# Optimization experiments

Measured on AMD Instinct MI355X. Metric: run time of the kernel, lower is better.

Reference implementation:

```python
import jax, jax.numpy as jnp
import numpy as np

MIN_MAP = jnp.array([-3.602826, -3.602826, -3.602826], dtype=jnp.float32)

def _conv(x, w, stride, pad):
    return jax.lax.conv_general_dilated(x, w, (stride, stride), [(pad, pad), (pad, pad)],
                                        dimension_numbers=('NCHW', 'OIHW', 'NCHW'))

def _bn(x, g, b):
    # inference BatchNorm with running_mean=0, running_var=1 -> pure channel affine
    return x * g[None, :, None, None] + b[None, :, None, None]

def _maxpool2(x):
    return jax.lax.reduce_window(x, -jnp.inf, jax.lax.max, (1, 1, 2, 2), (1, 1, 2, 2), 'VALID')

def _rotations(angles):
    # angles: [N,3] (already multiplied by pi); matrix entries copied verbatim from the torch source
    c, s = jnp.cos(angles), jnp.sin(angles)
    z = jnp.zeros_like(c[:, 0]); o = jnp.ones_like(c[:, 0])
    Rx = jnp.stack([jnp.stack([o, z, z], -1),
                    jnp.stack([z, c[:, 0], s[:, 0]], -1),
                    jnp.stack([z, -s[:, 0], c[:, 0]], -1)], 1)
    Ry = jnp.stack([jnp.stack([c[:, 1], z, -s[:, 1]], -1),
                    jnp.stack([z, o, z], -1),
                    jnp.stack([s[:, 1], z, c[:, 1]], -1)], 1)
    Rz = jnp.stack([jnp.stack([c[:, 2], s[:, 2], z], -1),
                    jnp.stack([-s[:, 2], c[:, 2], z], -1),
                    jnp.stack([z, z, o], -1)], 1)
    return jnp.einsum('nij,njk,nkl->nil', Rx, Ry, Rz)  # [N,3,3]


def setup_inputs() -> dict:
    key = jax.random.key(0)
    ks = jax.random.split(key, 16)
    N, C, T, V, M = 32, 3, 224, 224, 2
    OC = 128
    def he(k, shape, fan_in):
        return jax.random.normal(k, shape, jnp.float32) * np.float32(np.sqrt(2.0 / fan_in))
    inp = {}
    inp['x'] = jax.random.normal(ks[0], (N, C, T, V, M), jnp.float32)
    inp['w1'] = he(ks[1], (OC, C, 5, 5), C * 25); inp['b1'] = jnp.zeros((OC,), jnp.float32)
    inp['g1'] = jnp.ones((OC,), jnp.float32); inp['be1'] = jnp.zeros((OC,), jnp.float32)
    inp['w2'] = he(ks[2], (OC, OC, 5, 5), OC * 25); inp['b2'] = jnp.zeros((OC,), jnp.float32)
    inp['g2'] = jnp.ones((OC,), jnp.float32); inp['be2'] = jnp.zeros((OC,), jnp.float32)
    feat = OC * (224 // 8) * (224 // 8)  # 100352
    inp['fw'] = jax.random.normal(ks[3], (6, feat), jnp.float32) * np.float32(np.sqrt(1.0 / feat))
    inp['fb'] = jnp.zeros((6,), jnp.float32)
    chans = [3, 64, 256, 512, 1024, 2048]  # surrogate ResNet-50-style /32 backbone
    for i in range(5):
        cin, cout = chans[i], chans[i + 1]
        inp['bw%d' % (i + 1)] = he(ks[4 + i], (cout, cin, 3, 3), cin * 9)
        inp['bg%d' % (i + 1)] = jnp.ones((cout,), jnp.float32)
        inp['bb%d' % (i + 1)] = jnp.zeros((cout,), jnp.float32)
    lin = 2048 * 7 * 7
    inp['lw'] = jax.random.normal(ks[10], (60, lin), jnp.float32) * np.float32(np.sqrt(1.0 / lin))
    inp['lb'] = jnp.zeros((60,), jnp.float32)
    return inp


def reference(x, w1, b1, g1, be1, w2, b2, g2, be2, fw, fb,
              bw1, bg1, bb1, bw2, bg2, bb2, bw3, bg3, bb3, bw4, bg4, bb4, bw5, bg5, bb5,
              lw, lb):
    N = x.shape[0]
    def person(xp):  # xp: [N,3,T,V]
        h = jax.nn.relu(_bn(_conv(xp, w1, 2, 2) + b1[None, :, None, None], g1, be1))
        h = jax.nn.relu(_bn(_conv(h, w2, 2, 2) + b2[None, :, None, None], g2, be2))
        h = _maxpool2(h)                       # [N,128,28,28]
        o = h.reshape(N, -1) @ fw.T + fb       # [N,6]
        # torch builds rotations from out[n,:3].item() -> constants w.r.t. autodiff
        R = _rotations(jax.lax.stop_gradient(o[:, :3]) * jnp.pi)
        xf = xp.reshape(N, 3, -1)
        rot = jnp.einsum('nij,njk->nik', R, xf)
        shift = jnp.einsum('nij,nj->ni', R, MIN_MAP[None, :] - o[:, 3:])
        bias = 255.0 * (shift - MIN_MAP[None, :]) / 8.812765
        z = (rot + bias[:, :, None]).reshape(xp.shape)
        for w, g, b in ((bw1, bg1, bb1), (bw2, bg2, bb2), (bw3, bg3, bb3),
                        (bw4, bg4, bb4), (bw5, bg5, bb5)):
            z = jax.nn.relu(_bn(_conv(z, w, 2, 1), g, b))
        return z  # [N,2048,7,7]
    out = jnp.maximum(person(x[..., 0]), person(x[..., 1]))
    return out.reshape(N, -1) @ lw.T + lb  # [N,60]
```

## Files before the change

### kernel.cpp

```cpp
#include <hip/hip_runtime.h>
#include <hip/hip_bf16.h>

typedef unsigned short u16;
typedef __attribute__((ext_vector_type(8))) short bf16x8;
typedef __attribute__((ext_vector_type(4))) float f32x4;
typedef __attribute__((ext_vector_type(8))) unsigned short u16x8;
typedef __attribute__((ext_vector_type(4))) unsigned short u16x4;

__device__ __forceinline__ u16 f2bf(float v) {
    __hip_bfloat16 b = __float2bfloat16(v);
    return *reinterpret_cast<u16*>(&b);
}
__device__ __forceinline__ float bf2f(u16 u) {
    __hip_bfloat16 b;
    *reinterpret_cast<u16*>(&b) = u;
    return __bfloat162float(b);
}

__device__ __forceinline__ void gl_lds16(const u16* g, u16* l) {
    __builtin_amdgcn_global_load_lds(
        (const __attribute__((address_space(1))) void*)g,
        (__attribute__((address_space(3))) void*)l, 16, 0, 0);
}

__global__ void repack_w32(const float* __restrict__ w, u16* __restrict__ wh,
                           int Cout, int Cin, int KK) {
    int i = blockIdx.x * blockDim.x + threadIdx.x;
    int tot = Cout * Cin * KK;
    if (i >= tot) return;
    int oc = i / (Cin * KK);
    int r = i - oc * (Cin * KK);
    int p = r / Cin, ic = r - p * Cin;
    wh[(size_t)oc * (Cin * KK) + (size_t)p * Cin + ic] =
        f2bf(w[((size_t)oc * Cin + ic) * KK + p]);
}
__global__ void repack_split2(const float* __restrict__ w, u16* __restrict__ Ap,
                              int Cout, int CinR, int CinP, int KK, int Ksteps) {
    int cols = Ksteps * 64;
    int idx = blockIdx.x * blockDim.x + threadIdx.x;
    int tot = Cout * cols;
    if (idx >= tot) return;
    int oc = idx / cols, c = idx - oc * cols;
    int t = c >> 6, r = c & 63, half = r >> 5, j = r & 31;
    int kk = t * 32 + j;
    int p = kk / CinP, ic = kk - p * CinP;
    float v = (p < KK && ic < CinR) ? w[((size_t)oc * CinR + ic) * KK + p] : 0.f;
    u16 h = f2bf(v);
    Ap[idx] = half ? f2bf(v - bf2f(h)) : h;
}
__global__ void repack_g4_2(const float* __restrict__ w, u16* __restrict__ Ap,
                            int Cout, int CinR, int KS, int Ksteps) {
    int cols = Ksteps * 64;
    int idx = blockIdx.x * blockDim.x + threadIdx.x;
    int tot = Cout * cols;
    if (idx >= tot) return;
    int oc = idx / cols, c = idx - oc * cols;
    int t = c >> 6, r = c & 63, half = r >> 5, j = r & 31;
    int pix = j >> 2, ch = j & 3;
    float v = (pix < KS && ch < CinR)
                  ? w[(((size_t)oc * CinR + ch) * KS + t) * KS + pix] : 0.f;
    u16 h = f2bf(v);
    Ap[idx] = half ? f2bf(v - bf2f(h)) : h;
}
__global__ void repack_g4(const float* __restrict__ w, u16* __restrict__ Ap,
                          int Cout, int CinR, int KS, int Kpp) {
    int idx = blockIdx.x * blockDim.x + threadIdx.x;
    int tot = Cout * Kpp;
    if (idx >= tot) return;
    int oc = idx / Kpp, kk = idx - oc * Kpp;
    int ky = kk >> 5, r = kk & 31;
    int pix = r >> 2, ch = r & 3;
    float v = (pix < KS && ch < CinR)
                  ? w[(((size_t)oc * CinR + ch) * KS + ky) * KS + pix] : 0.f;
    Ap[idx] = f2bf(v);
}

__global__ void extract_person4(const float* __restrict__ x, float* __restrict__ X,
                                u16* __restrict__ X4, int m, int total) {
    int idx = blockIdx.x * blockDim.x + threadIdx.x;
    if (idx >= total) return;
    int n = idx / 50176;
    int p = idx - n * 50176;
    int y = p / 224, xx = p - y * 224;
    u16 h[4];
    h[3] = 0;
#pragma unroll
    for (int c = 0; c < 3; ++c) {
        float v = x[(((size_t)(n * 3 + c)) * 50176 + p) * 2 + m];
        X[((size_t)(n * 3 + c)) * 50176 + p] = v;
        h[c] = f2bf(v);
    }
    size_t o = (((size_t)n * 228 + y + 2) * 232 + xx + 2) * 4;
    *reinterpret_cast<u16x4*>(&X4[o]) = *reinterpret_cast<u16x4*>(h);
}

__global__ void zero_u16(u16* __restrict__ b, size_t n8) {
    size_t i = (size_t)blockIdx.x * blockDim.x + threadIdx.x;
    if (i >= n8) return;
    u16x8 z = {0, 0, 0, 0, 0, 0, 0, 0};
    *reinterpret_cast<u16x8*>(&b[i * 8]) = z;
}
__global__ void zero_halo(u16* __restrict__ buf, int Nn, int Hp, int Wp, int C,
                          int P, int H, int W) {
    int idx = blockIdx.x * blockDim.x + threadIdx.x;
    int tot = Nn * Hp * Wp;
    if (idx >= tot) return;
    int x = idx % Wp, t = idx / Wp, y = t % Hp;
    if (y >= P && y < P + H && x >= P && x < P + W) return;
    u16* p = buf + (size_t)idx * C;
    u16x8 z = {0, 0, 0, 0, 0, 0, 0, 0};
    for (int c = 0; c < C; c += 8) *reinterpret_cast<u16x8*>(&p[c]) = z;
}

template <int BM, int CT, bool SPLIT, int MOUT>
__global__ __launch_bounds__(256) void gconv(
    const u16* __restrict__ A, const u16* __restrict__ B,
    const float* __restrict__ cbias, const float* __restrict__ gam,
    const float* __restrict__ bet,
    u16* __restrict__ outp, float* __restrict__ outf,
    int Nblk, int NHW, int Ksteps, int KSP,
    int Cin, int Hp_i, int Wp_i, int KS,
    int Wout, int HWout,
    int Cout, int Hp_o, int Wp_o, int P_o) {
    constexpr int WAVES_M = (BM == 128) ? 2 : 1;
    constexpr int WM = BM / WAVES_M;
    constexpr int WN = 128 / (4 / WAVES_M);
    constexpr int FM = WM / 16, FN = WN / 16;
    constexpr int ACOLS = SPLIT ? 64 : 32;
    constexpr int AR = (BM * ACOLS * 2) / 4096;

    __shared__ __align__(16) u16 Asb[2][BM * ACOLS];
    __shared__ __align__(16) u16 Bsb[2][128 * 32];

    const int tid = threadIdx.x;
    const int lane = tid & 63, wv = tid >> 6;

    const int nwg = gridDim.x, orig = blockIdx.x;
    const int qq = nwg >> 3, rr = nwg & 7, xcd = orig & 7;
    const int L = (xcd < rr ? xcd * (qq + 1) : rr * (qq + 1) + (xcd - rr) * qq) + (orig >> 3);
    const int bn = L % Nblk;
    const int mid = L / Nblk;
    const int kc = mid % KSP;
    const int bm = mid / KSP;
    const int s0 = bn * 128, oc0 = bm * BM;

    const int nsteps = Ksteps;
    const int Arow = Ksteps * ACOLS;

    const u16* asrc[AR];
#pragma unroll
    for (int r = 0; r < AR; ++r) {
        int idx = r * 256 + tid;
        if constexpr (SPLIT) {
            int row = idx >> 3, slot = idx & 7;
            int c = slot ^ (row & 7);
            asrc[r] = A + (size_t)(oc0 + row) * Arow + c * 8;
        } else {
            int row = idx >> 2, slot = idx & 3;
            int q = slot ^ ((row >> 1) & 3);
            asrc[r] = A + (size_t)(oc0 + row) * Arow + q * 8;
        }
    }
    long brow[2];
#pragma unroll
    for (int r = 0; r < 2; ++r) {
        int idx = r * 256 + tid;
        int srow = idx >> 2;
        int q = (idx & 3) ^ ((idx >> 3) & 3);
        int s = s0 + srow;
        if (s > NHW - 1) s = NHW - 1;
        int n = s / HWout, pos = s - n * HWout;
        int oy = pos / Wout, ox = pos - oy * Wout;
        brow[r] = (((long)n * Hp_i + 2 * oy) * Wp_i + 2 * ox) * Cin + q * 8;
    }

    auto stage = [&](int buf, int t) {
        long ao = (long)t * ACOLS;
#pragma unroll
        for (int r = 0; r < AR; ++r)
            gl_lds16(asrc[r] + ao, &Asb[buf][(r * 256 + wv * 64) * 8]);
        long so;
        if constexpr (CT == 32) {
            int csn = Cin >> 5;
            int p = t / csn, cs = t - p * csn;
            int ky = p / KS, kx = p - ky * KS;
            so = (long)(ky * Wp_i + kx) * Cin + cs * 32;
        } else {
            so = (long)t * Wp_i * 4;
        }
#pragma unroll
        for (int r = 0; r < 2; ++r)
            gl_lds16(B + brow[r] + so, &Bsb[buf][(r * 256 + wv * 64) * 8]);
    };

    const int cl = lane & 15, oct = lane >> 4;
    const int octx = oct ^ ((cl >> 1) & 3);
    const int aslot = oct ^ (cl & 7);
    const int wm0 = (WAVES_M == 2) ? (wv & 1) * WM : 0;
    const int wn0 = (WAVES_M == 2) ? (wv >> 1) * WN : wv * WN;

    f32x4 acc[FM][FN] = {};

    const int cs_steps = nsteps / KSP;
    const int t0 = kc * cs_steps, t1 = t0 + cs_steps;

    stage(0, t0);
    __syncthreads();
    for (int t = t0; t < t1; ++t) {
        const int cur = (t - t0) & 1;
        if (t + 1 < t1) stage(cur ^ 1, t + 1);
        bf16x8 af[FM], bfr[FN];
#pragma unroll
        for (int mi = 0; mi < FM; ++mi) {
            if constexpr (SPLIT)
                af[mi] = *reinterpret_cast<const bf16x8*>(
                    &Asb[cur][(wm0 + mi * 16 + cl) * ACOLS + aslot * 8]);
            else
                af[mi] = *reinterpret_cast<const bf16x8*>(
                    &Asb[cur][(wm0 + mi * 16 + cl) * ACOLS + octx * 8]);
        }
#pragma unroll
        for (int ni = 0; ni < FN; ++ni)
            bfr[ni] = *reinterpret_cast<const bf16x8*>(
                &Bsb[cur][(wn0 + ni * 16 + cl) * 32 + octx * 8]);
#pragma unroll
        for (int mi = 0; mi < FM; ++mi)
#pragma unroll
            for (int ni = 0; ni < FN; ++ni)
                acc[mi][ni] = __builtin_amdgcn_mfma_f32_16x16x32_bf16(
                    af[mi], bfr[ni], acc[mi][ni], 0, 0, 0);
        if constexpr (SPLIT) {
            bf16x8 al[FM];
#pragma unroll
            for (int mi = 0; mi < FM; ++mi)
                al[mi] = *reinterpret_cast<const bf16x8*>(
                    &Asb[cur][(wm0 + mi * 16 + cl) * ACOLS + (aslot ^ 4) * 8]);
#pragma unroll
            for (int mi = 0; mi < FM; ++mi)
#pragma unroll
                for (int ni = 0; ni < FN; ++ni)
                    acc[mi][ni] = __builtin_amdgcn_mfma_f32_16x16x32_bf16(
                        al[mi], bfr[ni], acc[mi][ni], 0, 0, 0);
        }
        __syncthreads();
    }

#pragma unroll
    for (int ni = 0; ni < FN; ++ni) {
        int s = s0 + wn0 + ni * 16 + cl;
        if (s >= NHW) continue;
        int n = s / HWout, pos = s - n * HWout;
        int oy = pos / Wout, ox = pos - oy * Wout;
#pragma unroll
        for (int mi = 0; mi < FM; ++mi) {
            int oc = oc0 + wm0 + mi * 16 + oct * 4;
            if constexpr (MOUT == 3) {
                float* pf = outf + (size_t)kc * ((size_t)NHW * Cout);
#pragma unroll
                for (int r3 = 0; r3 < 4; ++r3)
                    pf[((size_t)n * Cout + oc + r3) * HWout + pos] = acc[mi][ni][r3];
            } else if constexpr (MOUT == 2) {
#pragma unroll
                for (int r3 = 0; r3 < 4; ++r3) {
                    float v = acc[mi][ni][r3];
                    if (cbias) v += cbias[oc + r3];
                    v = fmaf(v, gam[oc + r3], bet[oc + r3]);
                    v = fmaxf(v, 0.f);
                    outf[((size_t)n * Cout + oc + r3) * HWout + pos] = v;
                }
            } else {
                u16 hh[4];
#pragma unroll
                for (int r3 = 0; r3 < 4; ++r3) {
                    float v = acc[mi][ni][r3];
                    if (cbias) v += cbias[oc + r3];
                    v = fmaf(v, gam[oc + r3], bet[oc + r3]);
                    v = fmaxf(v, 0.f);
                    hh[r3] = f2bf(v);
                }
                size_t ob = (((size_t)n * Hp_o + oy + P_o) * Wp_o + ox + P_o) * Cout + oc;
                *reinterpret_cast<u16x4*>(&outp[ob]) = *reinterpret_cast<u16x4*>(hh);
            }
        }
    }
}

__global__ void ksum_nchw(const float* __restrict__ part, const float* __restrict__ gam,
                          const float* __restrict__ bet, float* __restrict__ out,
                          size_t tot, size_t str, int HWout, int Cout, int KSP) {
    size_t i = (size_t)blockIdx.x * blockDim.x + threadIdx.x;
    if (i >= tot) return;
    float s = 0.f;
    for (int kc = 0; kc < KSP; ++kc) s += part[kc * str + i];
    int oc = (int)((i / HWout) % Cout);
    out[i] = fmaxf(fmaf(s, gam[oc], bet[oc]), 0.f);
}
__global__ void ksum_nhwc(const float* __restrict__ part, const float* __restrict__ gam,
                          const float* __restrict__ bet, u16* __restrict__ outp,
                          int NHW, int HWout, int Wout, int Cout,
                          int Hp, int Wp, int P, int KSP, size_t str) {
    int ocq = Cout >> 2;
    int idx = blockIdx.x * blockDim.x + threadIdx.x;
    if (idx >= NHW * ocq) return;
    int s = idx / ocq;
    int oc = (idx - s * ocq) * 4;
    int n = s / HWout, pos = s - n * HWout;
    int oy = pos / Wout, ox = pos - oy * Wout;
    u16 hh[4];
#pragma unroll
    for (int j = 0; j < 4; ++j) {
        float v = 0.f;
        for (int kc = 0; kc < KSP; ++kc)
            v += part[kc * str + ((size_t)n * Cout + oc + j) * HWout + pos];
        v = fmaxf(fmaf(v, gam[oc + j], bet[oc + j]), 0.f);
        hh[j] = f2bf(v);
    }
    size_t ob = (((size_t)n * Hp + oy + P) * Wp + ox + P) * Cout + oc;
    *reinterpret_cast<u16x4*>(&outp[ob]) = *reinterpret_cast<u16x4*>(hh);
}

__global__ void maxpool2(const float* __restrict__ in, float* __restrict__ out,
                         int NC, int H, int W) {
    int Ho = H >> 1, Wo = W >> 1;
    size_t idx = (size_t)blockIdx.x * blockDim.x + threadIdx.x;
    size_t total = (size_t)NC * Ho * Wo;
    if (idx >= total) return;
    int ox = idx % Wo;
    size_t t = idx / Wo;
    int oy = t % Ho;
    int nc = t / Ho;
    const float* p = in + ((size_t)nc * H + oy * 2) * W + ox * 2;
    out[idx] = fmaxf(fmaxf(p[0], p[1]), fmaxf(p[W], p[W + 1]));
}

__global__ __launch_bounds__(256) void lin_part(
    const float* __restrict__ X, const float* __restrict__ W,
    float* __restrict__ partial, int K, int Kc, int Ncols, int Nn) {
    int c = blockIdx.x / Nn;
    int n = blockIdx.x - c * Nn;
    int lane = threadIdx.x & 63, wv = threadIdx.x >> 6;
    const float4* x4 = reinterpret_cast<const float4*>(X + (size_t)n * K + (size_t)c * Kc);
    int K4 = Kc >> 2;
    for (int j = wv; j < Ncols; j += 4) {
        const float4* w4 =
            reinterpret_cast<const float4*>(W + (size_t)j * K + (size_t)c * Kc);
        float s = 0.f;
        for (int k = lane; k < K4; k += 64) {
            float4 a = x4[k], b = w4[k];
            s = fmaf(a.x, b.x, s);
            s = fmaf(a.y, b.y, s);
            s = fmaf(a.z, b.z, s);
            s = fmaf(a.w, b.w, s);
        }
#pragma unroll
        for (int off = 32; off > 0; off >>= 1) s += __shfl_down(s, off, 64);
        if (lane == 0) partial[((size_t)c * Nn + n) * 64 + j] = s;
    }
}

__global__ void lin_reduce(const float* __restrict__ partial,
                           const float* __restrict__ bias, float* __restrict__ out,
                           int Ncols, int Nn, int nchunks) {
    int t = blockIdx.x * blockDim.x + threadIdx.x;
    if (t >= Nn * Ncols) return;
    int n = t / Ncols, j = t - n * Ncols;
    float s = bias[j];
    for (int c = 0; c < nchunks; ++c) s += partial[((size_t)c * Nn + n) * 64 + j];
    out[t] = s;
}

__global__ void make_rot(const float* __restrict__ o6, float* __restrict__ R,
                         float* __restrict__ bv, int Nc) {
    int n = threadIdx.x;
    if (n >= Nc) return;
    const float PI = 3.14159265358979323846f;
    float a0 = o6[n * 6 + 0] * PI, a1 = o6[n * 6 + 1] * PI, a2 = o6[n * 6 + 2] * PI;
    float c0 = cosf(a0), c1 = cosf(a1), c2 = cosf(a2);
    float s0 = sinf(a0), s1 = sinf(a1), s2 = sinf(a2);
    float Rx[9] = {1, 0, 0, 0, c0, s0, 0, -s0, c0};
    float Ry[9] = {c1, 0, -s1, 0, 1, 0, s1, 0, c1};
    float Rz[9] = {c2, s2, 0, -s2, c2, 0, 0, 0, 1};
    float M[9], Rm[9];
#pragma unroll
    for (int i = 0; i < 3; ++i)
#pragma unroll
        for (int j = 0; j < 3; ++j) {
            float acc = 0.f;
#pragma unroll
            for (int k = 0; k < 3; ++k) acc = fmaf(Ry[i * 3 + k], Rz[k * 3 + j], acc);
            M[i * 3 + j] = acc;
        }
#pragma unroll
    for (int i = 0; i < 3; ++i)
#pragma unroll
        for (int j = 0; j < 3; ++j) {
            float acc = 0.f;
#pragma unroll
            for (int k = 0; k < 3; ++k) acc = fmaf(Rx[i * 3 + k], M[k * 3 + j], acc);
            Rm[i * 3 + j] = acc;
        }
    const float MINV = -3.602826f;
    float v0 = MINV - o6[n * 6 + 3];
    float v1 = MINV - o6[n * 6 + 4];
    float v2 = MINV - o6[n * 6 + 5];
#pragma unroll
    for (int i = 0; i < 3; ++i) {
        float sh = Rm[i * 3 + 0] * v0 + Rm[i * 3 + 1] * v1 + Rm[i * 3 + 2] * v2;
        bv[n * 3 + i] = 255.f * (sh - MINV) / 8.812765f;
        R[n * 9 + i * 3 + 0] = Rm[i * 3 + 0];
        R[n * 9 + i * 3 + 1] = Rm[i * 3 + 1];
        R[n * 9 + i * 3 + 2] = Rm[i * 3 + 2];
    }
}

__global__ void rot_apply4(const float* __restrict__ X, const float* __restrict__ R,
                           const float* __restrict__ bv, u16* __restrict__ z,
                           int total) {
    int idx = blockIdx.x * blockDim.x + threadIdx.x;
    if (idx >= total) return;
    int n = idx / 50176;
    int p = idx - n * 50176;
    int y = p / 224, xx = p - y * 224;
    const float* xb = X + (size_t)n * 3 * 50176 + p;
    float x0 = xb[0], x1 = xb[50176], x2 = xb[(size_t)2 * 50176];
    u16 o[4];
#pragma unroll
    for (int i = 0; i < 3; ++i) {
        float v = fmaf(R[n * 9 + i * 3 + 0], x0,
                  fmaf(R[n * 9 + i * 3 + 1], x1,
                  fmaf(R[n * 9 + i * 3 + 2], x2, bv[n * 3 + i])));
        o[i] = f2bf(v);
    }
    o[3] = 0;
    size_t ob = (((size_t)n * 226 + y + 1) * 232 + xx + 1) * 4;
    *reinterpret_cast<u16x4*>(&z[ob]) = *reinterpret_cast<u16x4*>(o);
}

__global__ void copy_kernel(const float* __restrict__ a, float* __restrict__ o, size_t n) {
    size_t i = (size_t)blockIdx.x * blockDim.x + threadIdx.x;
    if (i < n) o[i] = a[i];
}
__global__ void max_kernel(const float* __restrict__ a, float* __restrict__ o, size_t n) {
    size_t i = (size_t)blockIdx.x * blockDim.x + threadIdx.x;
    if (i < n) o[i] = fmaxf(o[i], a[i]);
}

static inline int nblk(size_t total, int bs) { return (int)((total + bs - 1) / bs); }

extern "C" void kernel_launch(void* const* d_in, const int* in_sizes, int n_in,
                              void* d_out, int out_size, void* d_ws, size_t ws_size,
                              hipStream_t stream) {
    const float* x   = (const float*)d_in[0];
    const float* w1  = (const float*)d_in[1];
    const float* b1  = (const float*)d_in[2];
    const float* g1  = (const float*)d_in[3];
    const float* be1 = (const float*)d_in[4];
    const float* w2  = (const float*)d_in[5];
    const float* b2  = (const float*)d_in[6];
    const float* g2  = (const float*)d_in[7];
    const float* be2 = (const float*)d_in[8];
    const float* fw  = (const float*)d_in[9];
    const float* fb  = (const float*)d_in[10];
    const float* bw[5], *bg[5], *bb[5];
    for (int i = 0; i < 5; ++i) {
        bw[i] = (const float*)d_in[11 + 3 * i];
        bg[i] = (const float*)d_in[12 + 3 * i];
        bb[i] = (const float*)d_in[13 + 3 * i];
    }
    const float* lw = (const float*)d_in[26];
    const float* lb = (const float*)d_in[27];
    float* out = (float*)d_out;

    const int N = 32;
    const int BS = 256;
    const size_t S_Pp = 100352;

    const size_t E_X4 = (size_t)228 * 232 * 4;
    const size_t E_Z  = (size_t)226 * 232 * 4;
    const size_t E_B1 = (size_t)116 * 116 * 128;
    const size_t E_Zb2 = (size_t)114 * 114 * 64;
    const size_t E_Zb3 = (size_t)58 * 58 * 256;
    const size_t E_Zb4 = (size_t)30 * 30 * 512;
    const size_t E_Zb5 = (size_t)16 * 16 * 1024;

    const size_t slotC_B = E_Zb2 * 2;
    const size_t per_sample_B = 602112 + E_X4 * 2 + E_Z * 2 +
                                E_B1 * 2 + slotC_B + S_Pp * 4;
    const size_t apack_u16 = (size_t)128 * 320 + (size_t)128 * 6400 + (size_t)64 * 96 +
                             (size_t)256 * 576 + (size_t)512 * 2304 +
                             (size_t)1024 * 4608 + (size_t)2048 * 9216;
    const size_t fixed_B = (size_t)N * S_Pp * 4 + 131072 * 4 + 8192 + apack_u16 * 2 + 4096;

    int Nc = N;
    while (Nc > 1 && (size_t)Nc * per_sample_B + fixed_B > ws_size) Nc >>= 1;

    char* cur = (char*)d_ws;
    auto alf = [&](size_t n) { float* p = (float*)cur; cur += ((n + 3) & ~(size_t)3) * 4; return p; };
    auto alu = [&](size_t n) { u16* p = (u16*)cur; cur += ((n + 7) & ~(size_t)7) * 2; return p; };

    float* PM = alf((size_t)N * S_Pp);
    float* O6 = alf(256);
    float* Rm = alf(384);
    float* BV = alf(384);
    float* LP = alf(131072);
    u16* Ap1 = alu((size_t)128 * 320);
    u16* Ap2 = alu((size_t)128 * 6400);
    u16* Ab1 = alu((size_t)64 * 96);
    u16* Ab2 = alu((size_t)256 * 576);
    u16* Ab3 = alu((size_t)512 * 2304);
    u16* Ab4 = alu((size_t)1024 * 4608);
    u16* Ab5 = alu((size_t)2048 * 9216);

    float* X   = alf((size_t)Nc * 150528);
    u16* X4p   = alu((size_t)Nc * E_X4);
    u16* Z16p  = alu((size_t)Nc * E_Z);
    u16* B1p   = alu((size_t)Nc * E_B1);
    u16* Zb3   = B1p;
    u16* Zb4   = Zb3 + (size_t)Nc * E_Zb3;
    u16* Zb5   = Zb4 + (size_t)Nc * E_Zb4;
    u16* SLOTC = alu((size_t)Nc * slotC_B / 2);
    float* C2f = (float*)SLOTC;
    u16* Zb2   = SLOTC;
    float* PartF = (float*)SLOTC;
    float* Pp  = alf((size_t)Nc * S_Pp);

    repack_g4_2<<<nblk((size_t)128 * 320, BS), BS, 0, stream>>>(w1, Ap1, 128, 3, 5, 5);
    repack_split2<<<nblk((size_t)128 * 6400, BS), BS, 0, stream>>>(w2, Ap2, 128, 128, 128, 25, 100);
    repack_g4<<<nblk((size_t)64 * 96, BS), BS, 0, stream>>>(bw[0], Ab1, 64, 3, 3, 96);
    repack_w32<<<nblk((size_t)256 * 576, BS), BS, 0, stream>>>(bw[1], Ab2, 256, 64, 9);
    repack_w32<<<nblk((size_t)512 * 2304, BS), BS, 0, stream>>>(bw[2], Ab3, 512, 256, 9);
    repack_w32<<<nblk((size_t)1024 * 4608, BS), BS, 0, stream>>>(bw[3], Ab4, 1024, 512, 9);
    repack_w32<<<nblk((size_t)2048 * 9216, BS), BS, 0, stream>>>(bw[4], Ab5, 2048, 1024, 9);

    zero_u16<<<nblk((size_t)Nc * E_X4 / 8, BS), BS, 0, stream>>>(X4p, (size_t)Nc * E_X4 / 8);
    zero_u16<<<nblk((size_t)Nc * E_Z / 8, BS), BS, 0, stream>>>(Z16p, (size_t)Nc * E_Z / 8);

    const int NHW1 = Nc * 12544;
    const int Nb1 = (NHW1 + 127) / 128;
    const int NHW2 = Nc * 3136;
    const int Nb2 = (NHW2 + 127) / 128;
    const int NHW3 = Nc * 784;
    const int Nb3 = (NHW3 + 127) / 128;
    const int NHW4 = Nc * 196;
    const int Nb4 = (NHW4 + 127) / 128;
    const int NHW5 = Nc * 49;
    const int Nb5 = (NHW5 + 127) / 128;
    const size_t str4 = (size_t)NHW4 * 1024;
    const size_t str5 = (size_t)NHW5 * 2048;

    for (int m = 0; m < 2; ++m) {
        for (int c0 = 0; c0 < N; c0 += Nc) {
            const float* xc = x + (size_t)c0 * 150528 * 2;
            int nNP = Nc * 50176;
            extract_person4<<<nblk(nNP, BS), BS, 0, stream>>>(xc, X, X4p, m, nNP);

            zero_halo<<<nblk((size_t)Nc * 116 * 116, BS), BS, 0, stream>>>(B1p, Nc, 116, 116, 128, 2, 112, 112);

            gconv<128, 4, true, 0><<<Nb1, 256, 0, stream>>>(
                Ap1, X4p, b1, g1, be1, B1p, nullptr,
                Nb1, NHW1, 5, 1, 4, 228, 232, 5, 112, 12544, 128, 116, 116, 2);
            gconv<128, 32, true, 2><<<Nb2, 256, 0, stream>>>(
                Ap2, B1p, b2, g2, be2, nullptr, C2f,
                Nb2, NHW2, 100, 1, 128, 116, 116, 5, 56, 3136, 128, 0, 0, 0);

            size_t nP = (size_t)Nc * S_Pp;
            maxpool2<<<nblk(nP, BS), BS, 0, stream>>>(C2f, Pp, Nc * 128, 56, 56);
            lin_part<<<64 * Nc, 256, 0, stream>>>(Pp, fw, LP, 100352, 1568, 6, Nc);
            lin_reduce<<<nblk(Nc * 6, 64), 64, 0, stream>>>(LP, fb, O6, 6, Nc, 64);
            make_rot<<<1, 64, 0, stream>>>(O6, Rm, BV, Nc);
            rot_apply4<<<nblk(nNP, BS), BS, 0, stream>>>(X, Rm, BV, Z16p, nNP);

            zero_halo<<<nblk((size_t)Nc * 114 * 114, BS), BS, 0, stream>>>(Zb2, Nc, 114, 114, 64, 1, 112, 112);
            zero_halo<<<nblk((size_t)Nc * 58 * 58, BS), BS, 0, stream>>>(Zb3, Nc, 58, 58, 256, 1, 56, 56);
            zero_halo<<<nblk((size_t)Nc * 30 * 30, BS), BS, 0, stream>>>(Zb4, Nc, 30, 30, 512, 1, 28, 28);
            zero_halo<<<nblk((size_t)Nc * 16 * 16, BS), BS, 0, stream>>>(Zb5, Nc, 16, 16, 1024, 1, 14, 14);

            gconv<64, 4, false, 0><<<Nb1, 256, 0, stream>>>(
                Ab1, Z16p, nullptr, bg[0], bb[0], Zb2, nullptr,
                Nb1, NHW1, 3, 1, 4, 226, 232, 3, 112, 12544, 64, 114, 114, 1);
            gconv<128, 32, false, 0><<<2 * Nb2, 256, 0, stream>>>(
                Ab2, Zb2, nullptr, bg[1], bb[1], Zb3, nullptr,
                Nb2, NHW2, 18, 1, 64, 114, 114, 3, 56, 3136, 256, 58, 58, 1);
            gconv<128, 32, false, 0><<<4 * Nb3, 256, 0, stream>>>(
                Ab3, Zb3, nullptr, bg[2], bb[2], Zb4, nullptr,
                Nb3, NHW3, 72, 1, 256, 58, 58, 3, 28, 784, 512, 30, 30, 1);
            gconv<128, 32, false, 3><<<8 * 2 * Nb4, 256, 0, stream>>>(
                Ab4, Zb4, nullptr, nullptr, nullptr, nullptr, PartF,
                Nb4, NHW4, 144, 2, 512, 30, 30, 3, 14, 196, 1024, 0, 0, 0);
            ksum_nhwc<<<nblk((size_t)NHW4 * 256, BS), BS, 0, stream>>>(
                PartF, bg[3], bb[3], Zb5, NHW4, 196, 14, 1024, 16, 16, 1, 2, str4);
            gconv<128, 32, false, 3><<<16 * 4 * Nb5, 256, 0, stream>>>(
                Ab5, Zb5, nullptr, nullptr, nullptr, nullptr, PartF,
                Nb5, NHW5, 288, 4, 1024, 16, 16, 3, 7, 49, 2048, 0, 0, 0);
            ksum_nchw<<<nblk((size_t)NHW5 * 2048, BS), BS, 0, stream>>>(
                PartF, bg[4], bb[4], Pp, (size_t)NHW5 * 2048, str5, 49, 2048, 4);

            float* PMc = PM + (size_t)c0 * S_Pp;
            size_t nOut = (size_t)Nc * S_Pp;
            if (m == 0)
                copy_kernel<<<nblk(nOut, BS), BS, 0, stream>>>(Pp, PMc, nOut);
            else
                max_kernel<<<nblk(nOut, BS), BS, 0, stream>>>(Pp, PMc, nOut);
        }
    }

    lin_part<<<64 * N, 256, 0, stream>>>(PM, lw, LP, 100352, 1568, 60, N);
    lin_reduce<<<nblk(N * 60, 64), 64, 0, stream>>>(LP, lb, out, 60, N, 64);
}
```

Baseline: 2.094 ms.

## Fuse person-max into ksum, drop fp32 person copy, reorder conv tile mapping

Removes the intermediate fp32 per-person copy of the input: the rotation kernel now reads the strided original input directly. The final split-K reduction writes straight into the person-max buffer and takes the max for the second person, which eliminates the separate copy/max kernels. The gconv block index decomposition is reordered so that consecutive workgroups on an XCD share the same N tile across M and K-split blocks, changing which data is reused in cache. The strided input reads in the rotation kernel are less coalesced.

```diff
diff --git a/kernel.cpp b/kernel.cpp
--- a/kernel.cpp
+++ b/kernel.cpp
@@ -75,7 +75,7 @@
     Ap[idx] = f2bf(v);
 }
 
-__global__ void extract_person4(const float* __restrict__ x, float* __restrict__ X,
+__global__ void extract_person4(const float* __restrict__ x,
                                 u16* __restrict__ X4, int m, int total) {
     int idx = blockIdx.x * blockDim.x + threadIdx.x;
     if (idx >= total) return;
@@ -85,11 +85,8 @@
     u16 h[4];
     h[3] = 0;
 #pragma unroll
-    for (int c = 0; c < 3; ++c) {
-        float v = x[(((size_t)(n * 3 + c)) * 50176 + p) * 2 + m];
-        X[((size_t)(n * 3 + c)) * 50176 + p] = v;
-        h[c] = f2bf(v);
-    }
+    for (int c = 0; c < 3; ++c)
+        h[c] = f2bf(x[(((size_t)(n * 3 + c)) * 50176 + p) * 2 + m]);
     size_t o = (((size_t)n * 228 + y + 2) * 232 + xx + 2) * 4;
     *reinterpret_cast<u16x4*>(&X4[o]) = *reinterpret_cast<u16x4*>(h);
 }
@@ -138,10 +135,12 @@
     const int nwg = gridDim.x, orig = blockIdx.x;
     const int qq = nwg >> 3, rr = nwg & 7, xcd = orig & 7;
     const int L = (xcd < rr ? xcd * (qq + 1) : rr * (qq + 1) + (xcd - rr) * qq) + (orig >> 3);
-    const int bn = L % Nblk;
-    const int mid = L / Nblk;
-    const int kc = mid % KSP;
-    const int bm = mid / KSP;
+    const int gmK = nwg / Nblk;
+    const int gm = gmK / KSP;
+    const int bn = L / gmK;
+    const int midK = L - bn * gmK;
+    const int bm = midK % gm;
+    const int kc = midK / gm;
     const int s0 = bn * 128, oc0 = bm * BM;
 
     const int nsteps = Ksteps;
@@ -287,13 +286,15 @@
 
 __global__ void ksum_nchw(const float* __restrict__ part, const float* __restrict__ gam,
                           const float* __restrict__ bet, float* __restrict__ out,
-                          size_t tot, size_t str, int HWout, int Cout, int KSP) {
+                          size_t tot, size_t str, int HWout, int Cout, int KSP,
+                          int domax) {
     size_t i = (size_t)blockIdx.x * blockDim.x + threadIdx.x;
     if (i >= tot) return;
     float s = 0.f;
     for (int kc = 0; kc < KSP; ++kc) s += part[kc * str + i];
     int oc = (int)((i / HWout) % Cout);
-    out[i] = fmaxf(fmaf(s, gam[oc], bet[oc]), 0.f);
+    float v = fmaxf(fmaf(s, gam[oc], bet[oc]), 0.f);
+    out[i] = domax ? fmaxf(out[i], v) : v;
 }
 __global__ void ksum_nhwc(const float* __restrict__ part, const float* __restrict__ gam,
                           const float* __restrict__ bet, u16* __restrict__ outp,
@@ -413,16 +414,17 @@
     }
 }
 
-__global__ void rot_apply4(const float* __restrict__ X, const float* __restrict__ R,
+__global__ void rot_apply5(const float* __restrict__ xc, const float* __restrict__ R,
                            const float* __restrict__ bv, u16* __restrict__ z,
-                           int total) {
+                           int m, int total) {
     int idx = blockIdx.x * blockDim.x + threadIdx.x;
     if (idx >= total) return;
     int n = idx / 50176;
     int p = idx - n * 50176;
     int y = p / 224, xx = p - y * 224;
-    const float* xb = X + (size_t)n * 3 * 50176 + p;
-    float x0 = xb[0], x1 = xb[50176], x2 = xb[(size_t)2 * 50176];
+    float x0 = xc[(((size_t)(n * 3 + 0)) * 50176 + p) * 2 + m];
+    float x1 = xc[(((size_t)(n * 3 + 1)) * 50176 + p) * 2 + m];
+    float x2 = xc[(((size_t)(n * 3 + 2)) * 50176 + p) * 2 + m];
     u16 o[4];
 #pragma unroll
     for (int i = 0; i < 3; ++i) {
@@ -434,15 +436,6 @@
     o[3] = 0;
     size_t ob = (((size_t)n * 226 + y + 1) * 232 + xx + 1) * 4;
     *reinterpret_cast<u16x4*>(&z[ob]) = *reinterpret_cast<u16x4*>(o);
-}
-
-__global__ void copy_kernel(const float* __restrict__ a, float* __restrict__ o, size_t n) {
-    size_t i = (size_t)blockIdx.x * blockDim.x + threadIdx.x;
-    if (i < n) o[i] = a[i];
-}
-__global__ void max_kernel(const float* __restrict__ a, float* __restrict__ o, size_t n) {
-    size_t i = (size_t)blockIdx.x * blockDim.x + threadIdx.x;
-    if (i < n) o[i] = fmaxf(o[i], a[i]);
 }
 
 static inline int nblk(size_t total, int bs) { return (int)((total + bs - 1) / bs); }
@@ -484,7 +477,7 @@
     const size_t E_Zb5 = (size_t)16 * 16 * 1024;
 
     const size_t slotC_B = E_Zb2 * 2;
-    const size_t per_sample_B = 602112 + E_X4 * 2 + E_Z * 2 +
+    const size_t per_sample_B = E_X4 * 2 + E_Z * 2 +
                                 E_B1 * 2 + slotC_B + S_Pp * 4;
     const size_t apack_u16 = (size_t)128 * 320 + (size_t)128 * 6400 + (size_t)64 * 96 +
                              (size_t)256 * 576 + (size_t)512 * 2304 +
@@ -511,7 +504,6 @@
     u16* Ab4 = alu((size_t)1024 * 4608);
     u16* Ab5 = alu((size_t)2048 * 9216);
 
-    float* X   = alf((size_t)Nc * 150528);
     u16* X4p   = alu((size_t)Nc * E_X4);
     u16* Z16p  = alu((size_t)Nc * E_Z);
     u16* B1p   = alu((size_t)Nc * E_B1);
@@ -552,7 +544,7 @@
         for (int c0 = 0; c0 < N; c0 += Nc) {
             const float* xc = x + (size_t)c0 * 150528 * 2;
             int nNP = Nc * 50176;
-            extract_person4<<<nblk(nNP, BS), BS, 0, stream>>>(xc, X, X4p, m, nNP);
+            extract_person4<<<nblk(nNP, BS), BS, 0, stream>>>(xc, X4p, m, nNP);
 
             zero_halo<<<nblk((size_t)Nc * 116 * 116, BS), BS, 0, stream>>>(B1p, Nc, 116, 116, 128, 2, 112, 112);
 
@@ -568,7 +560,7 @@
             lin_part<<<64 * Nc, 256, 0, stream>>>(Pp, fw, LP, 100352, 1568, 6, Nc);
             lin_reduce<<<nblk(Nc * 6, 64), 64, 0, stream>>>(LP, fb, O6, 6, Nc, 64);
             make_rot<<<1, 64, 0, stream>>>(O6, Rm, BV, Nc);
-            rot_apply4<<<nblk(nNP, BS), BS, 0, stream>>>(X, Rm, BV, Z16p, nNP);
+            rot_apply5<<<nblk(nNP, BS), BS, 0, stream>>>(xc, Rm, BV, Z16p, m, nNP);
 
             zero_halo<<<nblk((size_t)Nc * 114 * 114, BS), BS, 0, stream>>>(Zb2, Nc, 114, 114, 64, 1, 112, 112);
             zero_halo<<<nblk((size_t)Nc * 58 * 58, BS), BS, 0, stream>>>(Zb3, Nc, 58, 58, 256, 1, 56, 56);
@@ -592,15 +584,9 @@
             gconv<128, 32, false, 3><<<16 * 4 * Nb5, 256, 0, stream>>>(
                 Ab5, Zb5, nullptr, nullptr, nullptr, nullptr, PartF,
                 Nb5, NHW5, 288, 4, 1024, 16, 16, 3, 7, 49, 2048, 0, 0, 0);
+            float* PMc = PM + (size_t)c0 * S_Pp;
             ksum_nchw<<<nblk((size_t)NHW5 * 2048, BS), BS, 0, stream>>>(
-                PartF, bg[4], bb[4], Pp, (size_t)NHW5 * 2048, str5, 49, 2048, 4);
-
-            float* PMc = PM + (size_t)c0 * S_Pp;
-            size_t nOut = (size_t)Nc * S_Pp;
-            if (m == 0)
-                copy_kernel<<<nblk(nOut, BS), BS, 0, stream>>>(Pp, PMc, nOut);
-            else
-                max_kernel<<<nblk(nOut, BS), BS, 0, stream>>>(Pp, PMc, nOut);
+                PartF, bg[4], bb[4], PMc, (size_t)NHW5 * 2048, str5, 49, 2048, 4, m);
         }
     }
 
```

Result: no change. 2.060 ms (-1.6%).
